# Kernel tuning notes

Measured on AMD Instinct MI355X. Metric: run time of the kernel, lower is better.

Reference implementation:

```python
import jax, jax.numpy as jnp
import numpy as np

PROCESS_INIT = 1.0
OBSERVATION_INIT = 1.0


def _build_dynamics_A(K, fut_len):
    # shift-structured single-modal A: state slot i takes value of slot i+1, last step repeats
    sd = 2 * fut_len
    a = np.zeros((sd, sd), dtype=np.float32)
    for i in range(fut_len - 1):
        a[2 * i, 2 * i + 2] = 1.0
        a[2 * i + 1, 2 * i + 3] = 1.0
    a[sd - 2, sd - 2] = 1.0
    a[sd - 1, sd - 1] = 1.0
    # block-diagonal over K modes
    return jnp.asarray(np.kron(np.eye(K, dtype=np.float32), a))


def setup_inputs() -> dict:
    key = jax.random.key(0)
    ks = jax.random.split(key, 6)
    B, A, K, fut_len = 2, 32, 6, 30
    D = K * 2 * fut_len  # 360
    belief_mean = jax.random.normal(ks[0], (B, A, D), dtype=jnp.float32)
    M = jax.random.normal(ks[1], (B, A, D, D), dtype=jnp.float32)
    # symmetric, SPD (eigenvalues ~ 2 +/- 0.2) so linear solves are well-posed
    belief_covariance = 0.003 * (M + jnp.swapaxes(M, -1, -2)) + 2.0 * jnp.eye(D, dtype=jnp.float32)
    observations = jax.random.normal(ks[2], (B, A, D), dtype=jnp.float32)
    rs = jax.random.uniform(ks[3], (B, A), dtype=jnp.float32)
    initialized = jax.random.bernoulli(ks[4], 0.7, (B, A))
    selected = jax.random.bernoulli(ks[5], 0.8, (B, A))
    return {
        "belief_mean": belief_mean,
        "belief_covariance": belief_covariance,
        "observations": observations,
        "rs": rs,
        "initialized": initialized,
        "selected": selected,
        "K": K,
        "fut_len": fut_len,
    }


def reference(belief_mean, belief_covariance, observations, rs, initialized, selected, K, fut_len):
    D = K * 2 * fut_len
    A = _build_dynamics_A(K, fut_len)  # [D, D], static sparse shift structure
    I = jnp.eye(D, dtype=belief_mean.dtype)
    r_obs = (rs + OBSERVATION_INIT)[..., None, None]  # [B, A, 1, 1]

    init_new = selected & (~initialized)  # first observation of agent
    upd = selected & initialized          # predict + Kalman update

    # --- initialization branch ---
    mean_init = observations
    cov_init = belief_covariance + r_obs * I

    # --- predict step: m <- A m ; P <- A P A^T + Q, Q = process_init * I ---
    m_pred = belief_mean @ A.T  # [B, A, D]
    P_pred = jnp.einsum('ij,bnjk,lk->bnil', A, belief_covariance, A) + PROCESS_INIT * I

    # --- update step (H = I): S = P + R ; Kg = P S^{-1} ---
    S = P_pred + r_obs * I
    Kg = P_pred @ jnp.linalg.inv(S)
    m_upd = m_pred + jnp.einsum('bnij,bnj->bni', Kg, observations - m_pred)
    P_upd = (I - Kg) @ P_pred

    # --- scatter the three branches back (masked merge) ---
    mean_out = jnp.where(init_new[..., None], mean_init,
               jnp.where(upd[..., None], m_upd, belief_mean))
    cov_out = jnp.where(init_new[..., None, None], cov_init,
              jnp.where(upd[..., None, None], P_upd, belief_covariance))
    initialized_out = initialized | selected
    return mean_out, cov_out, initialized_out
```

## Files before the change

### kernel.cpp

```cpp
#include <hip/hip_runtime.h>

#define D 360
#define NAG 64
#define NB 60
#define NPAN 6
#define COV_OFF (NAG * D)
#define INIT_OFF (COV_OFF + NAG * D * D)
#define RBOFF(par, ag, ct) ((((par) * NAG + (ag)) * 6 + (ct)) * 3600)

__device__ __forceinline__ int gshift(int i) {
    return ((i % 60) < 58) ? (i + 2) : i;
}

__global__ __launch_bounds__(384) void build_kernel(
    const float* __restrict__ P, const float* __restrict__ mean_in,
    const float* __restrict__ obs, const float* __restrict__ rs,
    const int* __restrict__ init_f, const int* __restrict__ sel_f,
    float* __restrict__ out, float* __restrict__ rb)
{
    const int by = blockIdx.x, ag = blockIdx.y, t = threadIdx.x;
    const bool ini = init_f[ag] != 0, sel = sel_f[ag] != 0;
    const float c = rs[ag] + 1.0f;
    if (by == 45) {
        if (t < D) {
            float v = (sel && !ini) ? obs[ag * D + t] : mean_in[ag * D + t];
            out[ag * D + t] = v;
        }
        if (t == 0) out[INIT_OFF + ag] = (ini || sel) ? 1.0f : 0.0f;
        return;
    }
    if (t >= D) return;
    const float* Pa = P + (size_t)ag * D * D;
    float* cov = out + COV_OFF + (size_t)ag * D * D;
    const int j = t;
    if (sel && ini) {
        const int gj = gshift(j);
        #pragma unroll
        for (int s = 0; s < 8; ++s) {
            const int i = by * 8 + s;
            float v = Pa[(size_t)gshift(i) * D + gj];
            if (i == j) v += 1.0f + c;
            cov[(size_t)i * D + j] = v;
            if (i < NB && j >= NB)
                rb[RBOFF(0, ag, j / NB) + i * NB + (j % NB)] = v;
        }
    } else if (sel) {
        #pragma unroll
        for (int s = 0; s < 8; ++s) {
            const int i = by * 8 + s;
            cov[(size_t)i * D + j] = Pa[(size_t)i * D + j] + ((i == j) ? c : 0.0f);
        }
    } else {
        #pragma unroll
        for (int s = 0; s < 8; ++s) {
            const int i = by * 8 + s;
            cov[(size_t)i * D + j] = Pa[(size_t)i * D + j];
        }
    }
}

__device__ __forceinline__ void inv4(float4& m0, float4& m1, float4& m2, float4& m3)
{
    float pv, f;
    pv = 1.0f / m0.x;
    m0.y *= pv; m0.z *= pv; m0.w *= pv; m0.x = pv;
    f = m1.x; m1.y = fmaf(-f, m0.y, m1.y); m1.z = fmaf(-f, m0.z, m1.z); m1.w = fmaf(-f, m0.w, m1.w); m1.x = -f * pv;
    f = m2.x; m2.y = fmaf(-f, m0.y, m2.y); m2.z = fmaf(-f, m0.z, m2.z); m2.w = fmaf(-f, m0.w, m2.w); m2.x = -f * pv;
    f = m3.x; m3.y = fmaf(-f, m0.y, m3.y); m3.z = fmaf(-f, m0.z, m3.z); m3.w = fmaf(-f, m0.w, m3.w); m3.x = -f * pv;
    pv = 1.0f / m1.y;
    m1.x *= pv; m1.z *= pv; m1.w *= pv; m1.y = pv;
    f = m0.y; m0.x = fmaf(-f, m1.x, m0.x); m0.z = fmaf(-f, m1.z, m0.z); m0.w = fmaf(-f, m1.w, m0.w); m0.y = -f * pv;
    f = m2.y; m2.x = fmaf(-f, m1.x, m2.x); m2.z = fmaf(-f, m1.z, m2.z); m2.w = fmaf(-f, m1.w, m2.w); m2.y = -f * pv;
    f = m3.y; m3.x = fmaf(-f, m1.x, m3.x); m3.z = fmaf(-f, m1.z, m3.z); m3.w = fmaf(-f, m1.w, m3.w); m3.y = -f * pv;
    pv = 1.0f / m2.z;
    m2.x *= pv; m2.y *= pv; m2.w *= pv; m2.z = pv;
    f = m0.z; m0.x = fmaf(-f, m2.x, m0.x); m0.y = fmaf(-f, m2.y, m0.y); m0.w = fmaf(-f, m2.w, m0.w); m0.z = -f * pv;
    f = m1.z; m1.x = fmaf(-f, m2.x, m1.x); m1.y = fmaf(-f, m2.y, m1.y); m1.w = fmaf(-f, m2.w, m1.w); m1.z = -f * pv;
    f = m3.z; m3.x = fmaf(-f, m2.x, m3.x); m3.y = fmaf(-f, m2.y, m3.y); m3.w = fmaf(-f, m2.w, m3.w); m3.z = -f * pv;
    pv = 1.0f / m3.w;
    m3.x *= pv; m3.y *= pv; m3.z *= pv; m3.w = pv;
    f = m0.w; m0.x = fmaf(-f, m3.x, m0.x); m0.y = fmaf(-f, m3.y, m0.y); m0.z = fmaf(-f, m3.z, m0.z); m0.w = -f * pv;
    f = m1.w; m1.x = fmaf(-f, m3.x, m1.x); m1.y = fmaf(-f, m3.y, m1.y); m1.z = fmaf(-f, m3.z, m1.z); m1.w = -f * pv;
    f = m2.w; m2.x = fmaf(-f, m3.x, m2.x); m2.y = fmaf(-f, m3.y, m2.y); m2.z = fmaf(-f, m3.z, m2.z); m2.w = -f * pv;
}

struct Slab {
    float4 v0, v1, v2, v3, v4, v5, v6, v7, v8, v9, v10, v11, v12, v13, v14;
};
template<int I> __device__ __forceinline__ float4& AT(Slab& s) {
    if constexpr (I == 0) return s.v0;   else if constexpr (I == 1) return s.v1;
    else if constexpr (I == 2) return s.v2;  else if constexpr (I == 3) return s.v3;
    else if constexpr (I == 4) return s.v4;  else if constexpr (I == 5) return s.v5;
    else if constexpr (I == 6) return s.v6;  else if constexpr (I == 7) return s.v7;
    else if constexpr (I == 8) return s.v8;  else if constexpr (I == 9) return s.v9;
    else if constexpr (I == 10) return s.v10; else if constexpr (I == 11) return s.v11;
    else if constexpr (I == 12) return s.v12; else if constexpr (I == 13) return s.v13;
    else return s.v14;
}
template<int Q = 0> __device__ __forceinline__ void slab_load(Slab& s, const float* src) {
    if constexpr (Q < 15) { AT<Q>(s) = *(const float4*)(src + 4 * Q); slab_load<Q + 1>(s, src); }
}
template<int Q = 0> __device__ __forceinline__ void slab_store(Slab& s, float* dst) {
    if constexpr (Q < 15) { *(float4*)(dst + 4 * Q) = AT<Q>(s); slab_store<Q + 1>(s, dst); }
}
template<int Q = 0> __device__ __forceinline__ void slab_stage(Slab& s, float4 (&dst)[15]) {
    if constexpr (Q < 15) { dst[Q] = AT<Q>(s); slab_stage<Q + 1>(s, dst); }
}
template<int KB, int Q = 0> __device__ __forceinline__ void zero_except(Slab& s) {
    if constexpr (Q < 15) {
        if constexpr (Q != KB) AT<Q>(s) = make_float4(0.f, 0.f, 0.f, 0.f);
        zero_except<KB, Q + 1>(s);
    }
}
template<int KB, int Q = 0>
__device__ __forceinline__ void rank4(Slab& s, const float4 sc, const float4 (&pb)[4][15]) {
    if constexpr (Q < 15) {
        if constexpr (Q != KB) {
            const float4 p0 = pb[0][Q], p1 = pb[1][Q], p2 = pb[2][Q], p3 = pb[3][Q];
            float4& r = AT<Q>(s);
            r.x = fmaf(sc.x, p0.x, fmaf(sc.y, p1.x, fmaf(sc.z, p2.x, fmaf(sc.w, p3.x, r.x))));
            r.y = fmaf(sc.x, p0.y, fmaf(sc.y, p1.y, fmaf(sc.z, p2.y, fmaf(sc.w, p3.y, r.y))));
            r.z = fmaf(sc.x, p0.z, fmaf(sc.y, p1.z, fmaf(sc.z, p2.z, fmaf(sc.w, p3.z, r.z))));
            r.w = fmaf(sc.x, p0.w, fmaf(sc.y, p1.w, fmaf(sc.z, p2.w, fmaf(sc.w, p3.w, r.w))));
        }
        rank4<KB, Q + 1>(s, sc, pb);
    }
}
template<int Q = 0>
__device__ __forceinline__ void slab_store_fin(Slab& s, float* dst, int r, int j0,
                                               float c, float c2) {
    if constexpr (Q < 15) {
        const int cg = j0 + 4 * Q;
        const float4 v = AT<Q>(s);
        float4 o;
        o.x = ((r == cg + 0) ? c : 0.f) - c2 * v.x;
        o.y = ((r == cg + 1) ? c : 0.f) - c2 * v.y;
        o.z = ((r == cg + 2) ? c : 0.f) - c2 * v.z;
        o.w = ((r == cg + 3) ? c : 0.f) - c2 * v.w;
        *(float4*)(dst + 4 * Q) = o;
        slab_store_fin<Q + 1>(s, dst, r, j0, c, c2);
    }
}

template<int KB>
__device__ __forceinline__ void gj_step(Slab& s, int r, int rel, float4 (&praw)[2][4][15])
{
    const int buf = KB & 1;
    float4 m0 = praw[buf][0][KB];
    float4 m1 = praw[buf][1][KB];
    float4 m2 = praw[buf][2][KB];
    float4 m3 = praw[buf][3][KB];
    inv4(m0, m1, m2, m3);
    if (r < D) {
        const bool is_piv = (rel >= 4 * KB) && (rel < 4 * KB + 4);
        float4 sc;
        if (is_piv) {
            const int i = rel - 4 * KB;
            sc = (i == 0) ? m0 : (i == 1) ? m1 : (i == 2) ? m2 : m3;
            zero_except<KB>(s);
        } else {
            const float4 fr = AT<KB>(s);
            sc.x = -(fr.x * m0.x + fr.y * m1.x + fr.z * m2.x + fr.w * m3.x);
            sc.y = -(fr.x * m0.y + fr.y * m1.y + fr.z * m2.y + fr.w * m3.y);
            sc.z = -(fr.x * m0.z + fr.y * m1.z + fr.z * m2.z + fr.w * m3.z);
            sc.w = -(fr.x * m0.w + fr.y * m1.w + fr.z * m2.w + fr.w * m3.w);
        }
        rank4<KB>(s, sc, praw[buf]);
        AT<KB>(s) = sc;
        if (KB < 14 && rel >= 4 * (KB + 1) && rel < 4 * (KB + 1) + 4) {
            slab_stage(s, praw[buf ^ 1][rel - 4 * (KB + 1)]);
        }
    }
    __syncthreads();
}

template<int KB> struct GJ {
    __device__ static __forceinline__ void run(Slab& s, int r, int rel,
                                               float4 (&praw)[2][4][15]) {
        gj_step<KB>(s, r, rel, praw);
        GJ<KB + 1>::run(s, r, rel, praw);
    }
};
template<> struct GJ<15> {
    __device__ static __forceinline__ void run(Slab&, int, int, float4 (&)[2][4][15]) {}
};

__global__ __launch_bounds__(384) void factor_kernel(
    float* __restrict__ out, const float* __restrict__ rs,
    const int* __restrict__ init_f, const int* __restrict__ sel_f,
    float* __restrict__ rb, int p)
{
    const int ag = blockIdx.x;
    if (!(init_f[ag] && sel_f[ag])) return;
    float* M = out + COV_OFF + (size_t)ag * D * D;
    const int j0 = p * NB;
    const int r = threadIdx.x;
    const int rel = r - j0;
    Slab s;
    if (r < D) slab_load(s, M + (size_t)r * D + j0);
    __shared__ float4 praw[2][4][15];
    if (rel >= 0 && rel < 4) slab_stage(s, praw[0][rel]);
    __syncthreads();
    GJ<0>::run(s, r, rel, praw);
    if (r < D) {
        float* dst = M + (size_t)r * D + j0;
        if (p == NPAN - 1) {
            const float c = rs[ag] + 1.0f;
            slab_store_fin(s, dst, r, j0, c, c * c);
        } else {
            slab_store(s, dst);
            const int nrel = r - NB * (p + 1);
            if (nrel >= 0 && nrel < NB)
                slab_store(s, rb + RBOFF((p + 1) & 1, ag, p) + nrel * NB);
        }
    }
}

__device__ __forceinline__ void mm_row(const float4 a, const float4 b0, const float4 b1,
                                       const float4 b2, const float4 b3, float acc[4]) {
    acc[0] = fmaf(a.x, b0.x, fmaf(a.y, b1.x, fmaf(a.z, b2.x, fmaf(a.w, b3.x, acc[0]))));
    acc[1] = fmaf(a.x, b0.y, fmaf(a.y, b1.y, fmaf(a.z, b2.y, fmaf(a.w, b3.y, acc[1]))));
    acc[2] = fmaf(a.x, b0.z, fmaf(a.y, b1.z, fmaf(a.z, b2.z, fmaf(a.w, b3.z, acc[2]))));
    acc[3] = fmaf(a.x, b0.w, fmaf(a.y, b1.w, fmaf(a.z, b2.w, fmaf(a.w, b3.w, acc[3]))));
}

__global__ __launch_bounds__(256) void update_kernel(
    float* __restrict__ out, const float* __restrict__ rs,
    const int* __restrict__ init_f, const int* __restrict__ sel_f,
    float* __restrict__ rb, int p)
{
    const int ag = blockIdx.x;
    if (!(init_f[ag] && sel_f[ag])) return;
    const int ct = blockIdx.y + (blockIdx.y >= p ? 1 : 0);
    float* M = out + COV_OFF + (size_t)ag * D * D;
    const int j0 = p * NB, c0 = ct * NB;
    const float c = rs[ag] + 1.0f;
    const float c2 = c * c;
    __shared__ float R[NB][NB + 8];
    __shared__ float F[NB][NB + 8];
    const int t = threadIdx.x;
    {
        const float* rsrc = rb + RBOFF(p & 1, ag, ct);
        for (int idx = t; idx < NB * 15; idx += 256) {
            int k = idx / 15, q = idx % 15;
            *(float4*)&R[k][4 * q] = *(const float4*)(rsrc + k * NB + 4 * q);
        }
    }
    const int tx = t % 16, ty = t / 16;
    for (int rr = 0; rr < 2; ++rr) {
        const int rt = (int)blockIdx.z * 2 + rr;
        const int r0 = rt * NB;
        __syncthreads();
        for (int idx = t; idx < NB * 15; idx += 256) {
            int rrw = idx / 15, q = idx % 15;
            float4 v = *(const float4*)(M + (size_t)(r0 + rrw) * D + j0 + 4 * q);
            if (p == NPAN - 1) {
                const int rg = r0 + rrw, cg = j0 + 4 * q;
                v.x = (((rg == cg + 0) ? c : 0.f) - v.x) / c2;
                v.y = (((rg == cg + 1) ? c : 0.f) - v.y) / c2;
                v.z = (((rg == cg + 2) ? c : 0.f) - v.z) / c2;
                v.w = (((rg == cg + 3) ? c : 0.f) - v.w) / c2;
            }
            *(float4*)&F[rrw][4 * q] = v;
        }
        __syncthreads();
        if (tx < 15 && ty < 15) {
            float acc[4][4];
            #pragma unroll
            for (int i = 0; i < 4; ++i)
                #pragma unroll
                for (int j = 0; j < 4; ++j) acc[i][j] = 0.0f;
            for (int kq = 0; kq < 15; ++kq) {
                float4 a0 = *(const float4*)&F[4 * ty + 0][4 * kq];
                float4 a1 = *(const float4*)&F[4 * ty + 1][4 * kq];
                float4 a2 = *(const float4*)&F[4 * ty + 2][4 * kq];
                float4 a3 = *(const float4*)&F[4 * ty + 3][4 * kq];
                float4 b0 = *(const float4*)&R[4 * kq + 0][4 * tx];
                float4 b1 = *(const float4*)&R[4 * kq + 1][4 * tx];
                float4 b2 = *(const float4*)&R[4 * kq + 2][4 * tx];
                float4 b3 = *(const float4*)&R[4 * kq + 3][4 * tx];
                mm_row(a0, b0, b1, b2, b3, acc[0]);
                mm_row(a1, b0, b1, b2, b3, acc[1]);
                mm_row(a2, b0, b1, b2, b3, acc[2]);
                mm_row(a3, b0, b1, b2, b3, acc[3]);
            }
            #pragma unroll
            for (int i = 0; i < 4; ++i) {
                const int rg = r0 + 4 * ty + i;
                float* dst = M + (size_t)rg * D + c0 + 4 * tx;
                float4 base;
                if (rt == p) { base = make_float4(0.f, 0.f, 0.f, 0.f); }
                else         { base = *(const float4*)dst; }
                float4 v;
                v.x = base.x + acc[i][0];
                v.y = base.y + acc[i][1];
                v.z = base.z + acc[i][2];
                v.w = base.w + acc[i][3];
                if (p < NPAN - 1) {
                    if (rt == p + 1 && ct != p + 1) {
                        float* rdst = rb + RBOFF((p + 1) & 1, ag, ct) + (4 * ty + i) * NB + 4 * tx;
                        *(float4*)rdst = v;
                    }
                    *(float4*)dst = v;
                } else {
                    const int cg = c0 + 4 * tx;
                    float4 o;
                    o.x = ((rg == cg + 0) ? c : 0.f) - c2 * v.x;
                    o.y = ((rg == cg + 1) ? c : 0.f) - c2 * v.y;
                    o.z = ((rg == cg + 2) ? c : 0.f) - c2 * v.z;
                    o.w = ((rg == cg + 3) ? c : 0.f) - c2 * v.w;
                    *(float4*)dst = o;
                }
            }
        }
    }
}

__global__ __launch_bounds__(384) void solve_mean_kernel(
    float* __restrict__ out, const float* __restrict__ mean_in,
    const float* __restrict__ obs, const float* __restrict__ rs,
    const int* __restrict__ init_f, const int* __restrict__ sel_f)
{
    const int ag = blockIdx.x;
    if (!(init_f[ag] && sel_f[ag])) return;
    const float* C = out + COV_OFF + (size_t)ag * D * D;
    __shared__ float dsh[D];
    const int t = threadIdx.x;
    if (t < D) dsh[t] = obs[ag * D + t] - mean_in[ag * D + gshift(t)];
    __syncthreads();
    if (t < D) {
        float dot = 0.0f;
        #pragma unroll 8
        for (int j = 0; j < D; ++j)
            dot = fmaf(C[(size_t)j * D + t], dsh[j], dot);
        const float c = rs[ag] + 1.0f;
        out[ag * D + t] = obs[ag * D + t] - dsh[t] + dot / c;
    }
}

extern "C" void kernel_launch(void* const* d_in, const int* in_sizes, int n_in,
                              void* d_out, int out_size, void* d_ws, size_t ws_size,
                              hipStream_t stream) {
    const float* mean_in     = (const float*)d_in[0];
    const float* P           = (const float*)d_in[1];
    const float* obs         = (const float*)d_in[2];
    const float* rs          = (const float*)d_in[3];
    const int*   initialized = (const int*)d_in[4];
    const int*   selected    = (const int*)d_in[5];
    float* out = (float*)d_out;
    float* rb  = (float*)d_ws;

    build_kernel<<<dim3(46, NAG), 384, 0, stream>>>(P, mean_in, obs, rs,
                                                    initialized, selected, out, rb);
    for (int p = 0; p < NPAN; ++p) {
        factor_kernel<<<NAG, 384, 0, stream>>>(out, rs, initialized, selected, rb, p);
        update_kernel<<<dim3(NAG, NPAN - 1, 3), 256, 0, stream>>>(out, rs, initialized,
                                                                  selected, rb, p);
    }
    solve_mean_kernel<<<NAG, 384, 0, stream>>>(out, mean_in, obs, rs, initialized, selected);
}
```

Measured before the change: 303.8 us.

## Widen blocked Gauss-Jordan panels to 120 columns, halving panel passes

Panel width grows from 60 to 120, so the blocked inversion runs 3 factor/update passes instead of 6. The factor kernel now keeps 30 float4 per thread in registers (launch bounds set to one block per CU), and the update kernel is re-tiled into 60x60 output tiles with a K depth of 120 over a 4x6 grid. The stash buffer layout is reorganised into 60-column slots to match. The goal is fewer kernel launches and less global traffic per pass, at the cost of much higher register pressure and possible spills in the factor kernel.

```diff
diff --git a/kernel.cpp b/kernel.cpp
--- a/kernel.cpp
+++ b/kernel.cpp
@@ -2,11 +2,11 @@
 
 #define D 360
 #define NAG 64
-#define NB 60
-#define NPAN 6
+#define NB 120
+#define NPAN 3
 #define COV_OFF (NAG * D)
 #define INIT_OFF (COV_OFF + NAG * D * D)
-#define RBOFF(par, ag, ct) ((((par) * NAG + (ag)) * 6 + (ct)) * 3600)
+#define SB(par, ag, slot) ((((size_t)(par) * NAG + (ag)) * 4 + (slot)) * 7200)
 
 __device__ __forceinline__ int gshift(int i) {
     return ((i % 60) < 58) ? (i + 2) : i;
@@ -42,7 +42,7 @@
             if (i == j) v += 1.0f + c;
             cov[(size_t)i * D + j] = v;
             if (i < NB && j >= NB)
-                rb[RBOFF(0, ag, j / NB) + i * NB + (j % NB)] = v;
+                rb[SB(0, ag, j / 60 - 2) + i * 60 + (j % 60)] = v;
         }
     } else if (sel) {
         #pragma unroll
@@ -84,8 +84,11 @@
     f = m2.w; m2.x = fmaf(-f, m3.x, m2.x); m2.y = fmaf(-f, m3.y, m2.y); m2.z = fmaf(-f, m3.z, m2.z); m2.w = -f * pv;
 }
 
+#define NQ 30
 struct Slab {
-    float4 v0, v1, v2, v3, v4, v5, v6, v7, v8, v9, v10, v11, v12, v13, v14;
+    float4 v0, v1, v2, v3, v4, v5, v6, v7, v8, v9,
+           v10, v11, v12, v13, v14, v15, v16, v17, v18, v19,
+           v20, v21, v22, v23, v24, v25, v26, v27, v28, v29;
 };
 template<int I> __device__ __forceinline__ float4& AT(Slab& s) {
     if constexpr (I == 0) return s.v0;   else if constexpr (I == 1) return s.v1;
@@ -95,26 +98,41 @@
     else if constexpr (I == 8) return s.v8;  else if constexpr (I == 9) return s.v9;
     else if constexpr (I == 10) return s.v10; else if constexpr (I == 11) return s.v11;
     else if constexpr (I == 12) return s.v12; else if constexpr (I == 13) return s.v13;
-    else return s.v14;
+    else if constexpr (I == 14) return s.v14; else if constexpr (I == 15) return s.v15;
+    else if constexpr (I == 16) return s.v16; else if constexpr (I == 17) return s.v17;
+    else if constexpr (I == 18) return s.v18; else if constexpr (I == 19) return s.v19;
+    else if constexpr (I == 20) return s.v20; else if constexpr (I == 21) return s.v21;
+    else if constexpr (I == 22) return s.v22; else if constexpr (I == 23) return s.v23;
+    else if constexpr (I == 24) return s.v24; else if constexpr (I == 25) return s.v25;
+    else if constexpr (I == 26) return s.v26; else if constexpr (I == 27) return s.v27;
+    else if constexpr (I == 28) return s.v28; else return s.v29;
 }
 template<int Q = 0> __device__ __forceinline__ void slab_load(Slab& s, const float* src) {
-    if constexpr (Q < 15) { AT<Q>(s) = *(const float4*)(src + 4 * Q); slab_load<Q + 1>(s, src); }
+    if constexpr (Q < NQ) { AT<Q>(s) = *(const float4*)(src + 4 * Q); slab_load<Q + 1>(s, src); }
 }
 template<int Q = 0> __device__ __forceinline__ void slab_store(Slab& s, float* dst) {
-    if constexpr (Q < 15) { *(float4*)(dst + 4 * Q) = AT<Q>(s); slab_store<Q + 1>(s, dst); }
-}
-template<int Q = 0> __device__ __forceinline__ void slab_stage(Slab& s, float4 (&dst)[15]) {
-    if constexpr (Q < 15) { dst[Q] = AT<Q>(s); slab_stage<Q + 1>(s, dst); }
+    if constexpr (Q < NQ) { *(float4*)(dst + 4 * Q) = AT<Q>(s); slab_store<Q + 1>(s, dst); }
+}
+template<int Q = 0> __device__ __forceinline__ void slab_stage(Slab& s, float4 (&dst)[NQ]) {
+    if constexpr (Q < NQ) { dst[Q] = AT<Q>(s); slab_stage<Q + 1>(s, dst); }
+}
+template<int Q = 0> __device__ __forceinline__ void slab_store_stash(
+    Slab& s, float* rb_base, size_t stride_slot, int nrel) {
+    if constexpr (Q < NQ) {
+        float* dst = rb_base + (Q >= 15 ? stride_slot : 0) + nrel * 60 + (Q % 15) * 4;
+        *(float4*)dst = AT<Q>(s);
+        slab_store_stash<Q + 1>(s, rb_base, stride_slot, nrel);
+    }
 }
 template<int KB, int Q = 0> __device__ __forceinline__ void zero_except(Slab& s) {
-    if constexpr (Q < 15) {
+    if constexpr (Q < NQ) {
         if constexpr (Q != KB) AT<Q>(s) = make_float4(0.f, 0.f, 0.f, 0.f);
         zero_except<KB, Q + 1>(s);
     }
 }
 template<int KB, int Q = 0>
-__device__ __forceinline__ void rank4(Slab& s, const float4 sc, const float4 (&pb)[4][15]) {
-    if constexpr (Q < 15) {
+__device__ __forceinline__ void rank4(Slab& s, const float4 sc, const float4 (&pb)[4][NQ]) {
+    if constexpr (Q < NQ) {
         if constexpr (Q != KB) {
             const float4 p0 = pb[0][Q], p1 = pb[1][Q], p2 = pb[2][Q], p3 = pb[3][Q];
             float4& r = AT<Q>(s);
@@ -129,7 +147,7 @@
 template<int Q = 0>
 __device__ __forceinline__ void slab_store_fin(Slab& s, float* dst, int r, int j0,
                                                float c, float c2) {
-    if constexpr (Q < 15) {
+    if constexpr (Q < NQ) {
         const int cg = j0 + 4 * Q;
         const float4 v = AT<Q>(s);
         float4 o;
@@ -143,7 +161,7 @@
 }
 
 template<int KB>
-__device__ __forceinline__ void gj_step(Slab& s, int r, int rel, float4 (&praw)[2][4][15])
+__device__ __forceinline__ void gj_step(Slab& s, int r, int rel, float4 (&praw)[2][4][NQ])
 {
     const int buf = KB & 1;
     float4 m0 = praw[buf][0][KB];
@@ -167,7 +185,7 @@
         }
         rank4<KB>(s, sc, praw[buf]);
         AT<KB>(s) = sc;
-        if (KB < 14 && rel >= 4 * (KB + 1) && rel < 4 * (KB + 1) + 4) {
+        if (KB < NQ - 1 && rel >= 4 * (KB + 1) && rel < 4 * (KB + 1) + 4) {
             slab_stage(s, praw[buf ^ 1][rel - 4 * (KB + 1)]);
         }
     }
@@ -176,16 +194,16 @@
 
 template<int KB> struct GJ {
     __device__ static __forceinline__ void run(Slab& s, int r, int rel,
-                                               float4 (&praw)[2][4][15]) {
+                                               float4 (&praw)[2][4][NQ]) {
         gj_step<KB>(s, r, rel, praw);
         GJ<KB + 1>::run(s, r, rel, praw);
     }
 };
-template<> struct GJ<15> {
-    __device__ static __forceinline__ void run(Slab&, int, int, float4 (&)[2][4][15]) {}
+template<> struct GJ<NQ> {
+    __device__ static __forceinline__ void run(Slab&, int, int, float4 (&)[2][4][NQ]) {}
 };
 
-__global__ __launch_bounds__(384) void factor_kernel(
+__global__ __launch_bounds__(384, 1) void factor_kernel(
     float* __restrict__ out, const float* __restrict__ rs,
     const int* __restrict__ init_f, const int* __restrict__ sel_f,
     float* __restrict__ rb, int p)
@@ -198,7 +216,7 @@
     const int rel = r - j0;
     Slab s;
     if (r < D) slab_load(s, M + (size_t)r * D + j0);
-    __shared__ float4 praw[2][4][15];
+    __shared__ float4 praw[2][4][NQ];
     if (rel >= 0 && rel < 4) slab_stage(s, praw[0][rel]);
     __syncthreads();
     GJ<0>::run(s, r, rel, praw);
@@ -210,8 +228,10 @@
         } else {
             slab_store(s, dst);
             const int nrel = r - NB * (p + 1);
-            if (nrel >= 0 && nrel < NB)
-                slab_store(s, rb + RBOFF((p + 1) & 1, ag, p) + nrel * NB);
+            if (nrel >= 0 && nrel < NB) {
+                float* rb_base = rb + SB((p + 1) & 1, ag, 2 * p);
+                slab_store_stash(s, rb_base, (size_t)7200, nrel);
+            }
         }
     }
 }
@@ -231,86 +251,87 @@
 {
     const int ag = blockIdx.x;
     if (!(init_f[ag] && sel_f[ag])) return;
-    const int ct = blockIdx.y + (blockIdx.y >= p ? 1 : 0);
+    const int y = blockIdx.y;
+    const int ct = y + (y >= 2 * p ? 2 : 0);
+    const int rt = blockIdx.z;
+    const int r0 = 60 * rt, c0 = 60 * ct;
+    const bool panelrow = ((rt >> 1) == p);
     float* M = out + COV_OFF + (size_t)ag * D * D;
-    const int j0 = p * NB, c0 = ct * NB;
     const float c = rs[ag] + 1.0f;
     const float c2 = c * c;
-    __shared__ float R[NB][NB + 8];
-    __shared__ float F[NB][NB + 8];
+    __shared__ float R[NB][60];
+    __shared__ float F[60][NB + 4];
     const int t = threadIdx.x;
     {
-        const float* rsrc = rb + RBOFF(p & 1, ag, ct);
-        for (int idx = t; idx < NB * 15; idx += 256) {
-            int k = idx / 15, q = idx % 15;
-            *(float4*)&R[k][4 * q] = *(const float4*)(rsrc + k * NB + 4 * q);
-        }
-    }
-    const int tx = t % 16, ty = t / 16;
-    for (int rr = 0; rr < 2; ++rr) {
-        const int rt = (int)blockIdx.z * 2 + rr;
-        const int r0 = rt * NB;
-        __syncthreads();
-        for (int idx = t; idx < NB * 15; idx += 256) {
-            int rrw = idx / 15, q = idx % 15;
-            float4 v = *(const float4*)(M + (size_t)(r0 + rrw) * D + j0 + 4 * q);
+        const float* rsrc = rb + SB(p & 1, ag, y);
+        for (int idx = t; idx < 120 * 15; idx += 256) {
+            const int k = idx / 15, q = idx % 15;
+            *(float4*)&R[k][4 * q] = *(const float4*)(rsrc + k * 60 + 4 * q);
+        }
+    }
+    {
+        for (int idx = t; idx < 60 * NQ; idx += 256) {
+            const int row = idx / NQ, q = idx % NQ;
+            float4 v = *(const float4*)(M + (size_t)(r0 + row) * D + p * NB + 4 * q);
             if (p == NPAN - 1) {
-                const int rg = r0 + rrw, cg = j0 + 4 * q;
+                const int rg = r0 + row, cg = p * NB + 4 * q;
                 v.x = (((rg == cg + 0) ? c : 0.f) - v.x) / c2;
                 v.y = (((rg == cg + 1) ? c : 0.f) - v.y) / c2;
                 v.z = (((rg == cg + 2) ? c : 0.f) - v.z) / c2;
                 v.w = (((rg == cg + 3) ? c : 0.f) - v.w) / c2;
             }
-            *(float4*)&F[rrw][4 * q] = v;
-        }
-        __syncthreads();
-        if (tx < 15 && ty < 15) {
-            float acc[4][4];
+            *(float4*)&F[row][4 * q] = v;
+        }
+    }
+    __syncthreads();
+    const int tx = t % 16, ty = t / 16;
+    if (tx < 15 && ty < 15) {
+        float acc[4][4];
+        #pragma unroll
+        for (int i = 0; i < 4; ++i)
             #pragma unroll
-            for (int i = 0; i < 4; ++i)
-                #pragma unroll
-                for (int j = 0; j < 4; ++j) acc[i][j] = 0.0f;
-            for (int kq = 0; kq < 15; ++kq) {
-                float4 a0 = *(const float4*)&F[4 * ty + 0][4 * kq];
-                float4 a1 = *(const float4*)&F[4 * ty + 1][4 * kq];
-                float4 a2 = *(const float4*)&F[4 * ty + 2][4 * kq];
-                float4 a3 = *(const float4*)&F[4 * ty + 3][4 * kq];
-                float4 b0 = *(const float4*)&R[4 * kq + 0][4 * tx];
-                float4 b1 = *(const float4*)&R[4 * kq + 1][4 * tx];
-                float4 b2 = *(const float4*)&R[4 * kq + 2][4 * tx];
-                float4 b3 = *(const float4*)&R[4 * kq + 3][4 * tx];
-                mm_row(a0, b0, b1, b2, b3, acc[0]);
-                mm_row(a1, b0, b1, b2, b3, acc[1]);
-                mm_row(a2, b0, b1, b2, b3, acc[2]);
-                mm_row(a3, b0, b1, b2, b3, acc[3]);
-            }
-            #pragma unroll
-            for (int i = 0; i < 4; ++i) {
-                const int rg = r0 + 4 * ty + i;
-                float* dst = M + (size_t)rg * D + c0 + 4 * tx;
-                float4 base;
-                if (rt == p) { base = make_float4(0.f, 0.f, 0.f, 0.f); }
-                else         { base = *(const float4*)dst; }
-                float4 v;
-                v.x = base.x + acc[i][0];
-                v.y = base.y + acc[i][1];
-                v.z = base.z + acc[i][2];
-                v.w = base.w + acc[i][3];
-                if (p < NPAN - 1) {
-                    if (rt == p + 1 && ct != p + 1) {
-                        float* rdst = rb + RBOFF((p + 1) & 1, ag, ct) + (4 * ty + i) * NB + 4 * tx;
-                        *(float4*)rdst = v;
-                    }
-                    *(float4*)dst = v;
-                } else {
-                    const int cg = c0 + 4 * tx;
-                    float4 o;
-                    o.x = ((rg == cg + 0) ? c : 0.f) - c2 * v.x;
-                    o.y = ((rg == cg + 1) ? c : 0.f) - c2 * v.y;
-                    o.z = ((rg == cg + 2) ? c : 0.f) - c2 * v.z;
-                    o.w = ((rg == cg + 3) ? c : 0.f) - c2 * v.w;
-                    *(float4*)dst = o;
+            for (int j = 0; j < 4; ++j) acc[i][j] = 0.0f;
+        for (int kq = 0; kq < NQ; ++kq) {
+            float4 a0 = *(const float4*)&F[4 * ty + 0][4 * kq];
+            float4 a1 = *(const float4*)&F[4 * ty + 1][4 * kq];
+            float4 a2 = *(const float4*)&F[4 * ty + 2][4 * kq];
+            float4 a3 = *(const float4*)&F[4 * ty + 3][4 * kq];
+            float4 b0 = *(const float4*)&R[4 * kq + 0][4 * tx];
+            float4 b1 = *(const float4*)&R[4 * kq + 1][4 * tx];
+            float4 b2 = *(const float4*)&R[4 * kq + 2][4 * tx];
+            float4 b3 = *(const float4*)&R[4 * kq + 3][4 * tx];
+            mm_row(a0, b0, b1, b2, b3, acc[0]);
+            mm_row(a1, b0, b1, b2, b3, acc[1]);
+            mm_row(a2, b0, b1, b2, b3, acc[2]);
+            mm_row(a3, b0, b1, b2, b3, acc[3]);
+        }
+        #pragma unroll
+        for (int i = 0; i < 4; ++i) {
+            const int rg = r0 + 4 * ty + i;
+            float* dst = M + (size_t)rg * D + c0 + 4 * tx;
+            float4 base;
+            if (panelrow) { base = make_float4(0.f, 0.f, 0.f, 0.f); }
+            else          { base = *(const float4*)dst; }
+            float4 v;
+            v.x = base.x + acc[i][0];
+            v.y = base.y + acc[i][1];
+            v.z = base.z + acc[i][2];
+            v.w = base.w + acc[i][3];
+            if (p < NPAN - 1) {
+                if ((rt >> 1) == p + 1 && (ct >> 1) != p + 1) {
+                    const int slot = ct - (ct > 2 * p + 3 ? 2 : 0);
+                    const int srow = rg - NB * (p + 1);
+                    *(float4*)(rb + SB((p + 1) & 1, ag, slot) + srow * 60 + 4 * tx) = v;
                 }
+                *(float4*)dst = v;
+            } else {
+                const int cg = c0 + 4 * tx;
+                float4 o;
+                o.x = ((rg == cg + 0) ? c : 0.f) - c2 * v.x;
+                o.y = ((rg == cg + 1) ? c : 0.f) - c2 * v.y;
+                o.z = ((rg == cg + 2) ? c : 0.f) - c2 * v.z;
+                o.w = ((rg == cg + 3) ? c : 0.f) - c2 * v.w;
+                *(float4*)dst = o;
             }
         }
     }
@@ -354,8 +375,8 @@
                                                     initialized, selected, out, rb);
     for (int p = 0; p < NPAN; ++p) {
         factor_kernel<<<NAG, 384, 0, stream>>>(out, rs, initialized, selected, rb, p);
-        update_kernel<<<dim3(NAG, NPAN - 1, 3), 256, 0, stream>>>(out, rs, initialized,
-                                                                  selected, rb, p);
+        update_kernel<<<dim3(NAG, 4, 6), 256, 0, stream>>>(out, rs, initialized,
+                                                           selected, rb, p);
     }
     solve_mean_kernel<<<NAG, 384, 0, stream>>>(out, mean_in, obs, rs, initialized, selected);
 }
```

Result: slower. 364.6 us (+20.0%).

## Split panel factorization into diagonal-block inverse plus parallel column-panel GEMM

Applied to the files above, without the earlier changes.

The per-panel Gauss-Jordan step, which swept all 360 rows of the column panel in one 384-thread block per agent, is split in two. A 64-thread kernel now inverts only the 60x60 diagonal block into workspace. A second kernel with 6 blocks per agent multiplies each row tile by that inverse to rebuild the column panel. This spreads the serial panel work over more blocks and turns most of it into GEMM, at the cost of one extra launch per panel and a workspace round trip.

```diff
diff --git a/kernel.cpp b/kernel.cpp
--- a/kernel.cpp
+++ b/kernel.cpp
@@ -7,6 +7,7 @@
 #define COV_OFF (NAG * D)
 #define INIT_OFF (COV_OFF + NAG * D * D)
 #define RBOFF(par, ag, ct) ((((par) * NAG + (ag)) * 6 + (ct)) * 3600)
+#define BVOFF(ag) (2764800 + (ag) * 3600)
 
 __device__ __forceinline__ int gshift(int i) {
     return ((i % 60) < 58) ? (i + 2) : i;
@@ -126,21 +127,6 @@
         rank4<KB, Q + 1>(s, sc, pb);
     }
 }
-template<int Q = 0>
-__device__ __forceinline__ void slab_store_fin(Slab& s, float* dst, int r, int j0,
-                                               float c, float c2) {
-    if constexpr (Q < 15) {
-        const int cg = j0 + 4 * Q;
-        const float4 v = AT<Q>(s);
-        float4 o;
-        o.x = ((r == cg + 0) ? c : 0.f) - c2 * v.x;
-        o.y = ((r == cg + 1) ? c : 0.f) - c2 * v.y;
-        o.z = ((r == cg + 2) ? c : 0.f) - c2 * v.z;
-        o.w = ((r == cg + 3) ? c : 0.f) - c2 * v.w;
-        *(float4*)(dst + 4 * Q) = o;
-        slab_store_fin<Q + 1>(s, dst, r, j0, c, c2);
-    }
-}
 
 template<int KB>
 __device__ __forceinline__ void gj_step(Slab& s, int r, int rel, float4 (&praw)[2][4][15])
@@ -185,35 +171,23 @@
     __device__ static __forceinline__ void run(Slab&, int, int, float4 (&)[2][4][15]) {}
 };
 
-__global__ __launch_bounds__(384) void factor_kernel(
-    float* __restrict__ out, const float* __restrict__ rs,
-    const int* __restrict__ init_f, const int* __restrict__ sel_f,
-    float* __restrict__ rb, int p)
+__global__ __launch_bounds__(64) void diag_inv_kernel(
+    const float* __restrict__ out, const int* __restrict__ init_f,
+    const int* __restrict__ sel_f, float* __restrict__ rb, int p)
 {
     const int ag = blockIdx.x;
     if (!(init_f[ag] && sel_f[ag])) return;
-    float* M = out + COV_OFF + (size_t)ag * D * D;
+    const float* M = out + COV_OFF + (size_t)ag * D * D;
     const int j0 = p * NB;
-    const int r = threadIdx.x;
-    const int rel = r - j0;
+    const int lane = threadIdx.x;
+    const int r = (lane < NB) ? lane : 999;
     Slab s;
-    if (r < D) slab_load(s, M + (size_t)r * D + j0);
+    if (lane < NB) slab_load(s, M + (size_t)(j0 + lane) * D + j0);
     __shared__ float4 praw[2][4][15];
-    if (rel >= 0 && rel < 4) slab_stage(s, praw[0][rel]);
+    if (lane < 4) slab_stage(s, praw[0][lane]);
     __syncthreads();
-    GJ<0>::run(s, r, rel, praw);
-    if (r < D) {
-        float* dst = M + (size_t)r * D + j0;
-        if (p == NPAN - 1) {
-            const float c = rs[ag] + 1.0f;
-            slab_store_fin(s, dst, r, j0, c, c * c);
-        } else {
-            slab_store(s, dst);
-            const int nrel = r - NB * (p + 1);
-            if (nrel >= 0 && nrel < NB)
-                slab_store(s, rb + RBOFF((p + 1) & 1, ag, p) + nrel * NB);
-        }
-    }
+    GJ<0>::run(s, r, lane, praw);
+    if (lane < NB) slab_store(s, rb + BVOFF(ag) + lane * NB);
 }
 
 __device__ __forceinline__ void mm_row(const float4 a, const float4 b0, const float4 b1,
@@ -222,6 +196,87 @@
     acc[1] = fmaf(a.x, b0.y, fmaf(a.y, b1.y, fmaf(a.z, b2.y, fmaf(a.w, b3.y, acc[1]))));
     acc[2] = fmaf(a.x, b0.z, fmaf(a.y, b1.z, fmaf(a.z, b2.z, fmaf(a.w, b3.z, acc[2]))));
     acc[3] = fmaf(a.x, b0.w, fmaf(a.y, b1.w, fmaf(a.z, b2.w, fmaf(a.w, b3.w, acc[3]))));
+}
+
+__global__ __launch_bounds__(256) void colpanel_kernel(
+    float* __restrict__ out, const float* __restrict__ rs,
+    const int* __restrict__ init_f, const int* __restrict__ sel_f,
+    float* __restrict__ rb, int p)
+{
+    const int ag = blockIdx.x;
+    if (!(init_f[ag] && sel_f[ag])) return;
+    const int rt = blockIdx.y;
+    float* M = out + COV_OFF + (size_t)ag * D * D;
+    const int j0 = p * NB, r0 = rt * NB;
+    const float c = rs[ag] + 1.0f;
+    const float c2 = c * c;
+    const bool ispnl = (rt == p);
+    __shared__ float Bsh[NB][64];
+    __shared__ float Csh[NB][64];
+    const int t = threadIdx.x;
+    for (int idx = t; idx < NB * 15; idx += 256) {
+        const int k = idx / 15, q = idx % 15;
+        *(float4*)&Bsh[k][4 * q] = *(const float4*)(rb + BVOFF(ag) + k * NB + 4 * q);
+    }
+    if (!ispnl) {
+        for (int idx = t; idx < NB * 15; idx += 256) {
+            const int i = idx / 15, q = idx % 15;
+            *(float4*)&Csh[i][4 * q] = *(const float4*)(M + (size_t)(r0 + i) * D + j0 + 4 * q);
+        }
+    }
+    __syncthreads();
+    const int tx = t % 16, ty = t / 16;
+    if (tx < 15 && ty < 15) {
+        float acc[4][4];
+        #pragma unroll
+        for (int i = 0; i < 4; ++i)
+            #pragma unroll
+            for (int j = 0; j < 4; ++j) acc[i][j] = 0.0f;
+        if (ispnl) {
+            #pragma unroll
+            for (int i = 0; i < 4; ++i)
+                #pragma unroll
+                for (int j = 0; j < 4; ++j) acc[i][j] = Bsh[4 * ty + i][4 * tx + j];
+        } else {
+            for (int kq = 0; kq < 15; ++kq) {
+                float4 a0 = *(const float4*)&Csh[4 * ty + 0][4 * kq];
+                float4 a1 = *(const float4*)&Csh[4 * ty + 1][4 * kq];
+                float4 a2 = *(const float4*)&Csh[4 * ty + 2][4 * kq];
+                float4 a3 = *(const float4*)&Csh[4 * ty + 3][4 * kq];
+                float4 b0 = *(const float4*)&Bsh[4 * kq + 0][4 * tx];
+                float4 b1 = *(const float4*)&Bsh[4 * kq + 1][4 * tx];
+                float4 b2 = *(const float4*)&Bsh[4 * kq + 2][4 * tx];
+                float4 b3 = *(const float4*)&Bsh[4 * kq + 3][4 * tx];
+                mm_row(a0, b0, b1, b2, b3, acc[0]);
+                mm_row(a1, b0, b1, b2, b3, acc[1]);
+                mm_row(a2, b0, b1, b2, b3, acc[2]);
+                mm_row(a3, b0, b1, b2, b3, acc[3]);
+            }
+            #pragma unroll
+            for (int i = 0; i < 4; ++i)
+                #pragma unroll
+                for (int j = 0; j < 4; ++j) acc[i][j] = -acc[i][j];
+        }
+        #pragma unroll
+        for (int i = 0; i < 4; ++i) {
+            const int rg = r0 + 4 * ty + i;
+            float4 v = make_float4(acc[i][0], acc[i][1], acc[i][2], acc[i][3]);
+            float* dst = M + (size_t)rg * D + j0 + 4 * tx;
+            if (p == NPAN - 1) {
+                const int cg = j0 + 4 * tx;
+                float4 o;
+                o.x = ((rg == cg + 0) ? c : 0.f) - c2 * v.x;
+                o.y = ((rg == cg + 1) ? c : 0.f) - c2 * v.y;
+                o.z = ((rg == cg + 2) ? c : 0.f) - c2 * v.z;
+                o.w = ((rg == cg + 3) ? c : 0.f) - c2 * v.w;
+                *(float4*)dst = o;
+            } else {
+                *(float4*)dst = v;
+                if (rt == p + 1)
+                    *(float4*)(rb + RBOFF((p + 1) & 1, ag, p) + (rg - NB * (p + 1)) * NB + 4 * tx) = v;
+            }
+        }
+    }
 }
 
 __global__ __launch_bounds__(256) void update_kernel(
@@ -242,8 +297,8 @@
     {
         const float* rsrc = rb + RBOFF(p & 1, ag, ct);
         for (int idx = t; idx < NB * 15; idx += 256) {
-            int k = idx / 15, q = idx % 15;
-            *(float4*)&R[k][4 * q] = *(const float4*)(rsrc + k * NB + 4 * q);
+            int k = idx / 15, qq = idx % 15;
+            *(float4*)&R[k][4 * qq] = *(const float4*)(rsrc + k * NB + 4 * qq);
         }
     }
     const int tx = t % 16, ty = t / 16;
@@ -252,16 +307,16 @@
         const int r0 = rt * NB;
         __syncthreads();
         for (int idx = t; idx < NB * 15; idx += 256) {
-            int rrw = idx / 15, q = idx % 15;
-            float4 v = *(const float4*)(M + (size_t)(r0 + rrw) * D + j0 + 4 * q);
+            int rrw = idx / 15, qq = idx % 15;
+            float4 v = *(const float4*)(M + (size_t)(r0 + rrw) * D + j0 + 4 * qq);
             if (p == NPAN - 1) {
-                const int rg = r0 + rrw, cg = j0 + 4 * q;
+                const int rg = r0 + rrw, cg = j0 + 4 * qq;
                 v.x = (((rg == cg + 0) ? c : 0.f) - v.x) / c2;
                 v.y = (((rg == cg + 1) ? c : 0.f) - v.y) / c2;
                 v.z = (((rg == cg + 2) ? c : 0.f) - v.z) / c2;
                 v.w = (((rg == cg + 3) ? c : 0.f) - v.w) / c2;
             }
-            *(float4*)&F[rrw][4 * q] = v;
+            *(float4*)&F[rrw][4 * qq] = v;
         }
         __syncthreads();
         if (tx < 15 && ty < 15) {
@@ -353,7 +408,9 @@
     build_kernel<<<dim3(46, NAG), 384, 0, stream>>>(P, mean_in, obs, rs,
                                                     initialized, selected, out, rb);
     for (int p = 0; p < NPAN; ++p) {
-        factor_kernel<<<NAG, 384, 0, stream>>>(out, rs, initialized, selected, rb, p);
+        diag_inv_kernel<<<NAG, 64, 0, stream>>>(out, initialized, selected, rb, p);
+        colpanel_kernel<<<dim3(NAG, 6), 256, 0, stream>>>(out, rs, initialized,
+                                                          selected, rb, p);
         update_kernel<<<dim3(NAG, NPAN - 1, 3), 256, 0, stream>>>(out, rs, initialized,
                                                                   selected, rb, p);
     }
```

Measured after the change: 307.5 us. No clear change (+1.2%).
